# Performance work log

Hardware: AMD Instinct MI355X
Metric: run time of the kernel (lower is better)

Reference implementation:

```python
import jax, jax.numpy as jnp
import numpy as np

NUM_HEADS = 16
ROPE_BASE = 10000.0
QK_GAIN_INIT = 12.0
EPS = 1e-6
# head_config = alternating ['rope','nope',...]; 1.0 -> RoPE applied to this head
ROPE_MASK = jnp.asarray(np.tile([1.0, 0.0], NUM_HEADS // 2), dtype=jnp.float32)


def setup_inputs() -> dict:
    key = jax.random.key(0)
    k0, k1, k2 = jax.random.split(key, 3)
    B, S, Dm = 2, 2048, 2048
    x = jax.random.normal(k0, (B, S, Dm), dtype=jnp.float32)
    # fused QKV projection and output projection (out_proj flagged zero-init in the
    # original; we use small random init so outputs/grads are non-trivial)
    w_qkv = jax.random.normal(k1, (Dm, 3 * Dm), dtype=jnp.float32) * (Dm ** -0.5)
    w_out = jax.random.normal(k2, (Dm, Dm), dtype=jnp.float32) * (Dm ** -0.5)
    q_gain = jnp.full((NUM_HEADS,), QK_GAIN_INIT, dtype=jnp.float32)
    return {"x": x, "w_qkv": w_qkv, "w_out": w_out, "q_gain": q_gain}


def _rope_cos_sin(seqlen, head_dim, dtype):
    half = head_dim // 2
    inv_freq = ROPE_BASE ** (-jnp.arange(0, half, dtype=jnp.float32) / half)
    theta = jnp.arange(seqlen, dtype=jnp.float32)[:, None] * inv_freq[None, :]  # [S, D/2]
    return jnp.cos(theta).astype(dtype), jnp.sin(theta).astype(dtype)


def _apply_rope(t, cos, sin):
    # t: [B, S, H, D]; cos/sin: [S, D/2] -> broadcast [1, S, 1, D/2]
    d2 = t.shape[-1] // 2
    t1, t2 = t[..., :d2], t[..., d2:]
    c = cos[None, :, None, :]
    s = sin[None, :, None, :]
    return jnp.concatenate([t1 * c - t2 * s, t1 * s + t2 * c], axis=-1)


def _unit_norm(t):
    # per-head-dim L2 normalization (qk-norm)
    return t * jax.lax.rsqrt(jnp.sum(t * t, axis=-1, keepdims=True) + EPS)


def reference(x, w_qkv, w_out, q_gain):
    B, S, Dm = x.shape
    H = NUM_HEADS
    D = Dm // H
    qkv = (x @ w_qkv).reshape(B, S, 3, H, D)
    q, k, v = qkv[:, :, 0], qkv[:, :, 1], qkv[:, :, 2]  # [B, S, H, D]
    q = _unit_norm(q)
    k = _unit_norm(k)
    cos, sin = _rope_cos_sin(S, D, x.dtype)
    m = ROPE_MASK[None, None, :, None]  # heterogeneous per-head dispatch
    q = m * _apply_rope(q, cos, sin) + (1.0 - m) * q
    k = m * _apply_rope(k, cos, sin) + (1.0 - m) * k
    # per-head learned qk gain instead of 1/sqrt(d)
    logits = jnp.einsum('bshd,bthd->bhst', q, k) * q_gain[None, :, None, None]
    causal = jnp.tril(jnp.ones((S, S), dtype=bool))
    logits = jnp.where(causal[None, None], logits, jnp.finfo(logits.dtype).min)
    attn = jax.nn.softmax(logits, axis=-1)
    y = jnp.einsum('bhst,bthd->bshd', attn, v).reshape(B, S, Dm)
    return y @ w_out
```

## Files before the change

kernel.cpp:

```cpp
#include <hip/hip_runtime.h>
#include <hip/hip_bf16.h>

typedef unsigned short ushort_t;
typedef __attribute__((ext_vector_type(8))) short short8;
typedef __attribute__((ext_vector_type(4))) float floatx4;

#define B_  2
#define S_  2048
#define DM_ 2048
#define H_  16
#define DH_ 128

#define AS1(p) ((const __attribute__((address_space(1))) void*)(p))
#define AS3(p) ((__attribute__((address_space(3))) void*)(p))

static __device__ __forceinline__ float b2f(ushort_t u) {
  __hip_bfloat16 h = *reinterpret_cast<__hip_bfloat16*>(&u);
  return __bfloat162float(h);
}
static __device__ __forceinline__ ushort_t f2b(float f) {
  __hip_bfloat16 h = __float2bfloat16(f);
  return *reinterpret_cast<ushort_t*>(&h);
}

__global__ __launch_bounds__(256) void convert_f32_bf16(const float* __restrict__ in,
                                                        ushort_t* __restrict__ out) {
  size_t i = ((size_t)blockIdx.x * 256 + threadIdx.x) * 8;
  float4 a = *(const float4*)(in + i);
  float4 b = *(const float4*)(in + i + 4);
  ushort_t tmp[8] = {f2b(a.x), f2b(a.y), f2b(a.z), f2b(a.w),
                     f2b(b.x), f2b(b.y), f2b(b.z), f2b(b.w)};
  *(uint4*)(out + i) = *(const uint4*)tmp;
}

__global__ __launch_bounds__(256) void transpose_f32_to_bf16T(const float* __restrict__ in,
                                                              ushort_t* __restrict__ out,
                                                              int R, int inC, int colOff) {
  __shared__ ushort_t tile[64][72];
  const int tid = threadIdx.x;
  const int r0 = blockIdx.y * 64, c0 = blockIdx.x * 64;
#pragma unroll
  for (int p = 0; p < 2; ++p) {
    int li = tid + p * 256;
    int r = li >> 3, cs = (li & 7) * 8;
    const float* src = in + (size_t)(r0 + r) * inC + colOff + c0 + cs;
    float4 a = *(const float4*)src;
    float4 b = *(const float4*)(src + 4);
    ushort_t tmp[8] = {f2b(a.x), f2b(a.y), f2b(a.z), f2b(a.w),
                       f2b(b.x), f2b(b.y), f2b(b.z), f2b(b.w)};
    *(uint4*)&tile[r][cs] = *(const uint4*)tmp;
  }
  __syncthreads();
#pragma unroll
  for (int p = 0; p < 2; ++p) {
    int li = tid + p * 256;
    int cR = li >> 3, rs = (li & 7) * 8;
    ushort_t tmp[8];
#pragma unroll
    for (int e = 0; e < 8; ++e) tmp[e] = tile[rs + e][cR];
    *(uint4*)(out + (size_t)(c0 + cR) * R + r0 + rs) = *(const uint4*)tmp;
  }
}

template <int MODE>
__global__ __launch_bounds__(256) void gemm_bt_async(const ushort_t* __restrict__ A,
                                                     const ushort_t* __restrict__ Bt,
                                                     void* __restrict__ C0,
                                                     void* __restrict__ C1,
                                                     int M, int N, int K) {
  __shared__ alignas(16) ushort_t As[2][128 * 32];
  __shared__ alignas(16) ushort_t Bs[2][128 * 32];
  const int tid = threadIdx.x;
  const int wave = tid >> 6, lane = tid & 63;
  const int l15 = lane & 15, quad = lane >> 4;
  const int wr = (wave >> 1) * 64, wc = (wave & 1) * 64;
  const int lin = blockIdx.y * gridDim.x + blockIdx.x;
  const int band = lin / (4 * gridDim.x);
  const int rin = lin % (4 * gridDim.x);
  const int by = band * 4 + (rin & 3);
  const int bx = rin >> 2;
  const size_t m0 = (size_t)by * 128, n0 = (size_t)bx * 128;
  const int srow = lane >> 2, scol = (lane & 3) * 8;

  floatx4 zero = {0.f, 0.f, 0.f, 0.f};
  floatx4 acc[4][4];
#pragma unroll
  for (int i = 0; i < 4; ++i)
#pragma unroll
    for (int j = 0; j < 4; ++j) acc[i][j] = zero;

  auto stage = [&](int kt, int bf) {
#pragma unroll
    for (int i = 0; i < 2; ++i) {
      int c = wave * 2 + i;
      int row = c * 16 + srow;
      __builtin_amdgcn_global_load_lds(AS1(A + (m0 + row) * K + kt + scol),
                                       AS3((char*)As[bf] + c * 1024), 16, 0, 0);
      __builtin_amdgcn_global_load_lds(AS1(Bt + (n0 + row) * K + kt + scol),
                                       AS3((char*)Bs[bf] + c * 1024), 16, 0, 0);
    }
  };

  stage(0, 0);
  const int niter = K / 32;
  for (int it = 0; it < niter; ++it) {
    const int cur = it & 1;
    __syncthreads();
    if (it + 1 < niter) stage((it + 1) * 32, cur ^ 1);

    short8 af[4], bfr[4];
#pragma unroll
    for (int i = 0; i < 4; ++i)
      af[i] = *(const short8*)&As[cur][(wr + i * 16 + l15) * 32 + quad * 8];
#pragma unroll
    for (int j = 0; j < 4; ++j)
      bfr[j] = *(const short8*)&Bs[cur][(wc + j * 16 + l15) * 32 + quad * 8];
#pragma unroll
    for (int i = 0; i < 4; ++i)
#pragma unroll
      for (int j = 0; j < 4; ++j)
        acc[i][j] = __builtin_amdgcn_mfma_f32_16x16x32_bf16(af[i], bfr[j], acc[i][j], 0, 0, 0);
  }

#pragma unroll
  for (int i = 0; i < 4; ++i)
#pragma unroll
    for (int j = 0; j < 4; ++j)
#pragma unroll
      for (int r = 0; r < 4; ++r) {
        size_t row = m0 + wr + i * 16 + quad * 4 + r;
        size_t col = n0 + wc + j * 16 + l15;
        if (MODE == 1)
          ((float*)C0)[row * N + col] = acc[i][j][r];
        else
          ((ushort_t*)C0)[row * N + col] = f2b(acc[i][j][r]);
      }
}

#define SBAR() __builtin_amdgcn_sched_barrier(0)
#define BARR() __builtin_amdgcn_s_barrier()

#define LDS_A(qm, bb)                                                          \
  _Pragma("unroll") for (int mi = 0; mi < 4; ++mi) {                           \
    _Pragma("unroll") for (int ks = 0; ks < 2; ++ks) {                         \
      const int r_ = arow + (qm) * 64 + mi * 16;                               \
      const int cb_ = ((ks) * 64 + quad * 16) ^ swz;                           \
      afr[qm][mi][ks] =                                                        \
          *(const short8*)((const char*)As[bb] + r_ * 128 + cb_);              \
    }                                                                          \
  }

#define LDS_B(qn, bb)                                                          \
  _Pragma("unroll") for (int ni = 0; ni < 2; ++ni) {                           \
    _Pragma("unroll") for (int ks = 0; ks < 2; ++ks) {                         \
      const int r_ = brow + (qn) * 32 + ni * 16;                               \
      const int cb_ = ((ks) * 64 + quad * 16) ^ swz;                           \
      bfr[qn][ni][ks] =                                                        \
          *(const short8*)((const char*)Bs[bb] + r_ * 128 + cb_);              \
    }                                                                          \
  }

#define MMA_Q(qm, qn)                                                          \
  _Pragma("unroll") for (int mi = 0; mi < 4; ++mi) {                           \
    _Pragma("unroll") for (int ni = 0; ni < 2; ++ni) {                         \
      floatx4 t_ = acc[(qm) * 4 + mi][(qn) * 2 + ni];                          \
      t_ = __builtin_amdgcn_mfma_f32_16x16x32_bf16(afr[qm][mi][0],             \
                                                   bfr[qn][ni][0], t_, 0, 0, 0); \
      t_ = __builtin_amdgcn_mfma_f32_16x16x32_bf16(afr[qm][mi][1],             \
                                                   bfr[qn][ni][1], t_, 0, 0, 0); \
      acc[(qm) * 4 + mi][(qn) * 2 + ni] = t_;                                  \
    }                                                                          \
  }

template <int MODE>
__global__ __launch_bounds__(512, 2) void gemm_bt_256(const ushort_t* __restrict__ A,
                                                      const ushort_t* __restrict__ Bt,
                                                      void* __restrict__ C0,
                                                      void* __restrict__ C1,
                                                      int M, int N, int K) {
  __shared__ alignas(16) ushort_t As[2][256 * 64];
  __shared__ alignas(16) ushort_t Bs[2][256 * 64];
  const int tid = threadIdx.x;
  const int wave = tid >> 6, lane = tid & 63;
  const int l15 = lane & 15, quad = lane >> 4;
  const int wm = wave >> 2, wn = wave & 3;
  const size_t m0 = (size_t)blockIdx.y * 256, n0 = (size_t)blockIdx.x * 256;
  const int nkt = K >> 6;

  const int srow = lane >> 3;
  const int skk = ((lane & 7) ^ srow) * 8;

  const int arow = wm * 128 + l15;
  const int brow = wn * 64 + l15;
  const int swz = (l15 & 7) << 4;

  floatx4 zero = {0.f, 0.f, 0.f, 0.f};
  floatx4 acc[8][4];
#pragma unroll
  for (int i = 0; i < 8; ++i)
#pragma unroll
    for (int j = 0; j < 4; ++j) acc[i][j] = zero;

  short8 afr[2][4][2];
  short8 bfr[2][2][2];

  auto stage_half = [&](int t, int ht) {
    if (t >= nkt) return;
    const int bb = t & 1;
    const int h = ht & 1;
    const int kt64 = t << 6;
    const ushort_t* G = (ht < 2) ? A : Bt;
    const size_t r0 = (ht < 2) ? m0 : n0;
    char* dst = (char*)((ht < 2) ? As[bb] : Bs[bb]) + h * 16384;
#pragma unroll
    for (int i = 0; i < 2; ++i) {
      const int c = wave * 2 + i;
      const size_t gr = r0 + h * 128 + c * 8 + srow;
      __builtin_amdgcn_global_load_lds(AS1(G + gr * K + kt64 + skk),
                                       AS3(dst + c * 1024), 16, 0, 0);
    }
  };

  stage_half(0, 0); stage_half(0, 1); stage_half(0, 2); stage_half(0, 3);
  stage_half(1, 0); stage_half(1, 1);
  SBAR();
  if (nkt > 1) { asm volatile("s_waitcnt vmcnt(4)" ::: "memory"); }
  else         { asm volatile("s_waitcnt vmcnt(0)" ::: "memory"); }
  SBAR(); BARR(); SBAR();

  for (int kt = 0; kt < nkt; ++kt) {
    const int bb = kt & 1;
    LDS_A(0, bb); LDS_B(0, bb);
    stage_half(kt + 1, 2);
    SBAR(); BARR(); SBAR();
    __builtin_amdgcn_s_setprio(1);
    MMA_Q(0, 0);
    __builtin_amdgcn_s_setprio(0);
    SBAR(); BARR(); SBAR();
    LDS_A(1, bb);
    stage_half(kt + 1, 3);
    SBAR(); BARR(); SBAR();
    __builtin_amdgcn_s_setprio(1);
    MMA_Q(1, 0);
    __builtin_amdgcn_s_setprio(0);
    SBAR(); BARR(); SBAR();
    LDS_B(1, bb);
    stage_half(kt + 2, 0);
    SBAR(); BARR(); SBAR();
    __builtin_amdgcn_s_setprio(1);
    MMA_Q(1, 1);
    __builtin_amdgcn_s_setprio(0);
    SBAR(); BARR(); SBAR();
    stage_half(kt + 2, 1);
    SBAR(); BARR(); SBAR();
    __builtin_amdgcn_s_setprio(1);
    MMA_Q(0, 1);
    __builtin_amdgcn_s_setprio(0);
    SBAR();
    if (kt + 2 < nkt) { asm volatile("s_waitcnt vmcnt(4)" ::: "memory"); }
    else              { asm volatile("s_waitcnt vmcnt(0)" ::: "memory"); }
    SBAR(); BARR(); SBAR();
  }

  if (MODE == 2) {
    ushort_t* Cb = (n0 >= 2048) ? (ushort_t*)C1 : (ushort_t*)C0;
    size_t nc0 = n0 & 2047;
#pragma unroll
    for (int mi8 = 0; mi8 < 8; ++mi8)
#pragma unroll
      for (int nj = 0; nj < 4; ++nj)
#pragma unroll
        for (int r = 0; r < 4; ++r) {
          size_t row = m0 + wm * 128 + (mi8 >> 2) * 64 + (mi8 & 3) * 16 + quad * 4 + r;
          size_t col = nc0 + wn * 64 + (nj >> 1) * 32 + (nj & 1) * 16 + l15;
          Cb[row * 2048 + col] = f2b(acc[mi8][nj][r]);
        }
  } else {
#pragma unroll
    for (int mi8 = 0; mi8 < 8; ++mi8)
#pragma unroll
      for (int nj = 0; nj < 4; ++nj)
#pragma unroll
        for (int r = 0; r < 4; ++r) {
          size_t row = m0 + wm * 128 + (mi8 >> 2) * 64 + (mi8 & 3) * 16 + quad * 4 + r;
          size_t col = n0 + wn * 64 + (nj >> 1) * 32 + (nj & 1) * 16 + l15;
          if (MODE == 1)
            ((float*)C0)[row * N + col] = acc[mi8][nj][r];
          else
            ((ushort_t*)C0)[row * N + col] = f2b(acc[mi8][nj][r]);
        }
  }
}

__global__ __launch_bounds__(256) void norm_rope(ushort_t* __restrict__ Q,
                                                 ushort_t* __restrict__ Kb,
                                                 const float* __restrict__ gain) {
  const int tid = threadIdx.x;
  const int wave = tid >> 6, lane = tid & 63;
  const int idx = blockIdx.x * 4 + wave;
  const int h = idx & 15;
  const int s = (idx >> 4) & (S_ - 1);
  const size_t off = (size_t)(idx >> 4) * DM_ + h * DH_;

  float q1 = b2f(Q[off + lane]),  q2 = b2f(Q[off + 64 + lane]);
  float k1 = b2f(Kb[off + lane]), k2 = b2f(Kb[off + 64 + lane]);

  float sq = q1 * q1 + q2 * q2;
  float sk = k1 * k1 + k2 * k2;
#pragma unroll
  for (int o = 1; o < 64; o <<= 1) {
    sq += __shfl_xor(sq, o, 64);
    sk += __shfl_xor(sk, o, 64);
  }
  float rq = rsqrtf(sq + 1e-6f), rk = rsqrtf(sk + 1e-6f);
  q1 *= rq; q2 *= rq; k1 *= rk; k2 *= rk;

  float qo1 = q1, qo2 = q2, ko1 = k1, ko2 = k2;
  if ((h & 1) == 0) {
    float invf = powf(10000.0f, -(float)lane * (1.0f / 64.0f));
    float th = (float)s * invf;
    float c = cosf(th), sn = sinf(th);
    qo1 = q1 * c - q2 * sn;  qo2 = q1 * sn + q2 * c;
    ko1 = k1 * c - k2 * sn;  ko2 = k1 * sn + k2 * c;
  }
  float g = gain[h];
  qo1 *= g; qo2 *= g;

  Q[off + lane]       = f2b(qo1);
  Q[off + 64 + lane]  = f2b(qo2);
  Kb[off + lane]      = f2b(ko1);
  Kb[off + 64 + lane] = f2b(ko2);
}

__global__ __launch_bounds__(256, 2) void attn(ushort_t* __restrict__ QY,
                                               const ushort_t* __restrict__ Kg,
                                               const ushort_t* __restrict__ Vg) {
  __shared__ alignas(16) ushort_t Ks[2][64 * 128];
  __shared__ alignas(16) ushort_t Vs[2][128 * 64];
  __shared__ alignas(16) ushort_t Ps[2][4][16 * 64];

  const float M0 = 13.0f;
  const int tid = threadIdx.x;
  const int wave = tid >> 6, lane = tid & 63;
  const int l15 = lane & 15, quad = lane >> 4;
  const int bh = blockIdx.y;
  const int b = bh >> 4, h = bh & 15;
  const int p = blockIdx.x;
  const int qt[2] = {p, 31 - p};

  const ushort_t* Kgb = Kg + (size_t)b * S_ * DM_ + h * DH_;
  const ushort_t* Vgb = Vg + (size_t)(h * DH_) * (B_ * S_) + b * S_;

  short8 aq[2][4];
#pragma unroll
  for (int t = 0; t < 2; ++t) {
    const ushort_t* Qg =
        QY + (size_t)(b * S_ + qt[t] * 64 + wave * 16 + l15) * DM_ + h * DH_;
#pragma unroll
    for (int ks = 0; ks < 4; ++ks)
      aq[t][ks] = *(const short8*)(Qg + ks * 32 + quad * 8);
  }

  float lsum[2][4] = {{0.f, 0.f, 0.f, 0.f}, {0.f, 0.f, 0.f, 0.f}};
  floatx4 zero = {0.f, 0.f, 0.f, 0.f};
  floatx4 oacc[2][8];
#pragma unroll
  for (int t = 0; t < 2; ++t)
#pragma unroll
    for (int d = 0; d < 8; ++d) oacc[t][d] = zero;

  const int krow_in = lane >> 4, ksd = lane & 15;
  const int vrow_in = lane >> 3, vsd = lane & 7;

  auto stage = [&](int kt, int bf) {
#pragma unroll
    for (int i = 0; i < 4; ++i) {
      int c = wave * 4 + i;
      {
        int r = c * 4 + krow_in;
        int sg = ksd ^ (r & 7);
        __builtin_amdgcn_global_load_lds(
            AS1(Kgb + (size_t)(kt * 64 + r) * DM_ + sg * 8),
            AS3((char*)Ks[bf] + c * 1024), 16, 0, 0);
      }
      {
        int r = c * 8 + vrow_in;
        int sg = vsd ^ (r & 7);
        __builtin_amdgcn_global_load_lds(
            AS1(Vgb + (size_t)r * (B_ * S_) + kt * 64 + sg * 8),
            AS3((char*)Vs[bf] + c * 1024), 16, 0, 0);
      }
    }
  };

  stage(0, 0);

  for (int kt = 0; kt <= qt[1]; ++kt) {
    const int cur = kt & 1;
    __syncthreads();
    if (kt < qt[1]) stage(kt + 1, cur ^ 1);

#pragma unroll
    for (int t = 0; t < 2; ++t) {
      if (t == 0 && kt > qt[0]) continue;
      floatx4 sacc[4];
#pragma unroll
      for (int j = 0; j < 4; ++j) sacc[j] = zero;
#pragma unroll
      for (int ks = 0; ks < 4; ++ks) {
#pragma unroll
        for (int j = 0; j < 4; ++j) {
          int row = j * 16 + l15;
          int sl = (ks * 4 + quad) ^ (row & 7);
          short8 bk = *(const short8*)&Ks[cur][row * 128 + sl * 8];
          sacc[j] = __builtin_amdgcn_mfma_f32_16x16x32_bf16(aq[t][ks], bk, sacc[j], 0, 0, 0);
        }
      }
      if (kt == qt[t]) {
#pragma unroll
        for (int j = 0; j < 4; ++j)
#pragma unroll
          for (int r = 0; r < 4; ++r) {
            int key = j * 16 + l15;
            int qr = wave * 16 + quad * 4 + r;
            if (key > qr) sacc[j][r] = -1e30f;
          }
      }
#pragma unroll
      for (int j = 0; j < 4; ++j)
#pragma unroll
        for (int r = 0; r < 4; ++r) {
          float pv = __expf(sacc[j][r] - M0);
          sacc[j][r] = pv;
          lsum[t][r] += pv;
        }
#pragma unroll
      for (int j = 0; j < 4; ++j)
#pragma unroll
        for (int r = 0; r < 4; ++r) {
          int row = quad * 4 + r;
          int col = j * 16 + l15;
          int g = col >> 3, w = col & 7;
          Ps[t][wave][row * 64 + ((g ^ (row & 7)) << 3) + w] = f2b(sacc[j][r]);
        }
#pragma unroll
      for (int ks2 = 0; ks2 < 2; ++ks2) {
        short8 ap = *(const short8*)&Ps[t][wave][l15 * 64 +
                                                (((ks2 * 4 + quad) ^ (l15 & 7)) << 3)];
#pragma unroll
        for (int d = 0; d < 8; ++d) {
          int row = d * 16 + l15;
          int sl = (ks2 * 4 + quad) ^ (row & 7);
          short8 bv = *(const short8*)&Vs[cur][row * 64 + sl * 8];
          oacc[t][d] = __builtin_amdgcn_mfma_f32_16x16x32_bf16(ap, bv, oacc[t][d], 0, 0, 0);
        }
      }
    }
  }

#pragma unroll
  for (int t = 0; t < 2; ++t) {
#pragma unroll
    for (int r = 0; r < 4; ++r) {
#pragma unroll
      for (int o = 1; o < 16; o <<= 1) lsum[t][r] += __shfl_xor(lsum[t][r], o, 64);
      float inv = 1.0f / lsum[t][r];
      size_t row = (size_t)(b * S_ + qt[t] * 64 + wave * 16 + quad * 4 + r);
#pragma unroll
      for (int d = 0; d < 8; ++d) {
        size_t col = (size_t)h * DH_ + d * 16 + l15;
        QY[row * DM_ + col] = f2b(oacc[t][d][r] * inv);
      }
    }
  }
}

extern "C" void kernel_launch(void* const* d_in, const int* in_sizes, int n_in,
                              void* d_out, int out_size, void* d_ws, size_t ws_size,
                              hipStream_t stream) {
  const float* x      = (const float*)d_in[0];
  const float* w_qkv  = (const float*)d_in[1];
  const float* w_out  = (const float*)d_in[2];
  const float* q_gain = (const float*)d_in[3];
  float* out = (float*)d_out;

  char* ws = (char*)d_ws;
  const size_t bsd = (size_t)B_ * S_ * DM_;
  ushort_t* Qraw = (ushort_t*)ws;
  ushort_t* Kraw = Qraw + bsd;
  ushort_t* Vt   = Kraw + bsd;
  ushort_t* wvT  = Vt + bsd;
  ushort_t* xbf  = (ushort_t*)d_out;
  ushort_t* wqkT = xbf + bsd;
  ushort_t* woutT = Kraw;

  convert_f32_bf16<<<dim3(bsd / (8 * 256)), 256, 0, stream>>>(x, xbf);
  transpose_f32_to_bf16T<<<dim3(64, 32), 256, 0, stream>>>(w_qkv, wqkT, DM_, 3 * DM_, 0);
  transpose_f32_to_bf16T<<<dim3(32, 32), 256, 0, stream>>>(w_qkv, wvT, DM_, 3 * DM_, 2 * DM_);

  gemm_bt_256<2><<<dim3(16, 16), 512, 0, stream>>>(xbf, wqkT, Qraw, Kraw,
                                                   B_ * S_, 2 * DM_, DM_);
  gemm_bt_async<0><<<dim3(32, 16), 256, 0, stream>>>(wvT, xbf, Vt, nullptr,
                                                     DM_, B_ * S_, DM_);
  norm_rope<<<dim3(B_ * S_ * H_ / 4), 256, 0, stream>>>(Qraw, Kraw, q_gain);
  attn<<<dim3(S_ / 128, B_ * H_), 256, 0, stream>>>(Qraw, Kraw, Vt);
  transpose_f32_to_bf16T<<<dim3(32, 32), 256, 0, stream>>>(w_out, woutT, DM_, DM_, 0);
  gemm_bt_async<1><<<dim3(16, 32), 256, 0, stream>>>(Qraw, woutT, out, nullptr,
                                                     B_ * S_, DM_, DM_);
}
```

Before: 392.4 us.

## Restage GEMM prefetch, vectorize norm_rope, use exp2 softmax, swap attn grid axes

The 256-tile GEMM now issues all four half-tile loads for the next k-step up front, waiting at vmcnt(8), and moves later stages into the third and fourth MMA phases. norm_rope handles four rows per wave with 4-wide vector loads and a 16-lane reduction. The log2(e) factor is folded into the q gain so attention can use a hardware exp2 with a rescaled max constant. The attention grid swaps its x and y axes so that heads sharing a query pair are scheduled next to each other.

```diff
diff --git a/kernel.cpp b/kernel.cpp
--- a/kernel.cpp
+++ b/kernel.cpp
@@ -21,6 +21,17 @@
 static __device__ __forceinline__ ushort_t f2b(float f) {
   __hip_bfloat16 h = __float2bfloat16(f);
   return *reinterpret_cast<ushort_t*>(&h);
+}
+static __device__ __forceinline__ float fast_exp2(float x) {
+#if defined(__has_builtin)
+#if __has_builtin(__builtin_amdgcn_exp2f)
+  return __builtin_amdgcn_exp2f(x);
+#else
+  return exp2f(x);
+#endif
+#else
+  return exp2f(x);
+#endif
 }
 
 __global__ __launch_bounds__(256) void convert_f32_bf16(const float* __restrict__ in,
@@ -222,42 +233,40 @@
   };
 
   stage_half(0, 0); stage_half(0, 1); stage_half(0, 2); stage_half(0, 3);
-  stage_half(1, 0); stage_half(1, 1);
+  stage_half(1, 0); stage_half(1, 1); stage_half(1, 2); stage_half(1, 3);
   SBAR();
-  if (nkt > 1) { asm volatile("s_waitcnt vmcnt(4)" ::: "memory"); }
+  if (nkt > 1) { asm volatile("s_waitcnt vmcnt(8)" ::: "memory"); }
   else         { asm volatile("s_waitcnt vmcnt(0)" ::: "memory"); }
   SBAR(); BARR(); SBAR();
 
   for (int kt = 0; kt < nkt; ++kt) {
     const int bb = kt & 1;
     LDS_A(0, bb); LDS_B(0, bb);
-    stage_half(kt + 1, 2);
     SBAR(); BARR(); SBAR();
     __builtin_amdgcn_s_setprio(1);
     MMA_Q(0, 0);
     __builtin_amdgcn_s_setprio(0);
     SBAR(); BARR(); SBAR();
     LDS_A(1, bb);
-    stage_half(kt + 1, 3);
     SBAR(); BARR(); SBAR();
     __builtin_amdgcn_s_setprio(1);
     MMA_Q(1, 0);
     __builtin_amdgcn_s_setprio(0);
     SBAR(); BARR(); SBAR();
     LDS_B(1, bb);
-    stage_half(kt + 2, 0);
+    stage_half(kt + 2, 0); stage_half(kt + 2, 1);
     SBAR(); BARR(); SBAR();
     __builtin_amdgcn_s_setprio(1);
     MMA_Q(1, 1);
     __builtin_amdgcn_s_setprio(0);
     SBAR(); BARR(); SBAR();
-    stage_half(kt + 2, 1);
+    stage_half(kt + 2, 2); stage_half(kt + 2, 3);
     SBAR(); BARR(); SBAR();
     __builtin_amdgcn_s_setprio(1);
     MMA_Q(0, 1);
     __builtin_amdgcn_s_setprio(0);
     SBAR();
-    if (kt + 2 < nkt) { asm volatile("s_waitcnt vmcnt(4)" ::: "memory"); }
+    if (kt + 2 < nkt) { asm volatile("s_waitcnt vmcnt(8)" ::: "memory"); }
     else              { asm volatile("s_waitcnt vmcnt(0)" ::: "memory"); }
     SBAR(); BARR(); SBAR();
   }
@@ -297,39 +306,55 @@
                                                  const float* __restrict__ gain) {
   const int tid = threadIdx.x;
   const int wave = tid >> 6, lane = tid & 63;
-  const int idx = blockIdx.x * 4 + wave;
+  const int g16 = lane >> 4, sl = lane & 15;
+  const int idx = (blockIdx.x * 4 + wave) * 4 + g16;
   const int h = idx & 15;
   const int s = (idx >> 4) & (S_ - 1);
-  const size_t off = (size_t)(idx >> 4) * DM_ + h * DH_;
-
-  float q1 = b2f(Q[off + lane]),  q2 = b2f(Q[off + 64 + lane]);
-  float k1 = b2f(Kb[off + lane]), k2 = b2f(Kb[off + 64 + lane]);
-
-  float sq = q1 * q1 + q2 * q2;
-  float sk = k1 * k1 + k2 * k2;
-#pragma unroll
-  for (int o = 1; o < 64; o <<= 1) {
+  const size_t off = (size_t)(idx >> 4) * DM_ + h * DH_ + sl * 4;
+
+  ushort_t qv1[4], qv2[4], kv1[4], kv2[4];
+  *(uint2*)qv1 = *(const uint2*)(Q + off);
+  *(uint2*)qv2 = *(const uint2*)(Q + off + 64);
+  *(uint2*)kv1 = *(const uint2*)(Kb + off);
+  *(uint2*)kv2 = *(const uint2*)(Kb + off + 64);
+
+  float q1[4], q2[4], k1[4], k2[4];
+  float sq = 0.f, sk = 0.f;
+#pragma unroll
+  for (int e = 0; e < 4; ++e) {
+    q1[e] = b2f(qv1[e]); q2[e] = b2f(qv2[e]);
+    k1[e] = b2f(kv1[e]); k2[e] = b2f(kv2[e]);
+    sq += q1[e] * q1[e] + q2[e] * q2[e];
+    sk += k1[e] * k1[e] + k2[e] * k2[e];
+  }
+#pragma unroll
+  for (int o = 1; o < 16; o <<= 1) {
     sq += __shfl_xor(sq, o, 64);
     sk += __shfl_xor(sk, o, 64);
   }
   float rq = rsqrtf(sq + 1e-6f), rk = rsqrtf(sk + 1e-6f);
-  q1 *= rq; q2 *= rq; k1 *= rk; k2 *= rk;
-
-  float qo1 = q1, qo2 = q2, ko1 = k1, ko2 = k2;
-  if ((h & 1) == 0) {
-    float invf = powf(10000.0f, -(float)lane * (1.0f / 64.0f));
-    float th = (float)s * invf;
-    float c = cosf(th), sn = sinf(th);
-    qo1 = q1 * c - q2 * sn;  qo2 = q1 * sn + q2 * c;
-    ko1 = k1 * c - k2 * sn;  ko2 = k1 * sn + k2 * c;
-  }
-  float g = gain[h];
-  qo1 *= g; qo2 *= g;
-
-  Q[off + lane]       = f2b(qo1);
-  Q[off + 64 + lane]  = f2b(qo2);
-  Kb[off + lane]      = f2b(ko1);
-  Kb[off + 64 + lane] = f2b(ko2);
+  const float g = gain[h] * 1.44269504f;
+  const bool roped = (h & 1) == 0;
+#pragma unroll
+  for (int e = 0; e < 4; ++e) {
+    float a = q1[e] * rq, bq = q2[e] * rq;
+    float c_ = k1[e] * rk, dk = k2[e] * rk;
+    if (roped) {
+      int j = sl * 4 + e;
+      float invf = exp2f((float)j * -0.20762050593f);
+      float th = (float)s * invf;
+      float cc = cosf(th), sn = sinf(th);
+      float na = a * cc - bq * sn, nb = a * sn + bq * cc;
+      float nc = c_ * cc - dk * sn, nd = c_ * sn + dk * cc;
+      a = na; bq = nb; c_ = nc; dk = nd;
+    }
+    qv1[e] = f2b(a * g); qv2[e] = f2b(bq * g);
+    kv1[e] = f2b(c_);    kv2[e] = f2b(dk);
+  }
+  *(uint2*)(Q + off)       = *(const uint2*)qv1;
+  *(uint2*)(Q + off + 64)  = *(const uint2*)qv2;
+  *(uint2*)(Kb + off)      = *(const uint2*)kv1;
+  *(uint2*)(Kb + off + 64) = *(const uint2*)kv2;
 }
 
 __global__ __launch_bounds__(256, 2) void attn(ushort_t* __restrict__ QY,
@@ -339,13 +364,13 @@
   __shared__ alignas(16) ushort_t Vs[2][128 * 64];
   __shared__ alignas(16) ushort_t Ps[2][4][16 * 64];
 
-  const float M0 = 13.0f;
+  const float M0 = 18.755035531f;
   const int tid = threadIdx.x;
   const int wave = tid >> 6, lane = tid & 63;
   const int l15 = lane & 15, quad = lane >> 4;
-  const int bh = blockIdx.y;
+  const int bh = blockIdx.x;
   const int b = bh >> 4, h = bh & 15;
-  const int p = blockIdx.x;
+  const int p = blockIdx.y;
   const int qt[2] = {p, 31 - p};
 
   const ushort_t* Kgb = Kg + (size_t)b * S_ * DM_ + h * DH_;
@@ -430,7 +455,7 @@
       for (int j = 0; j < 4; ++j)
 #pragma unroll
         for (int r = 0; r < 4; ++r) {
-          float pv = __expf(sacc[j][r] - M0);
+          float pv = fast_exp2(sacc[j][r] - M0);
           sacc[j][r] = pv;
           lsum[t][r] += pv;
         }
@@ -502,8 +527,8 @@
                                                    B_ * S_, 2 * DM_, DM_);
   gemm_bt_async<0><<<dim3(32, 16), 256, 0, stream>>>(wvT, xbf, Vt, nullptr,
                                                      DM_, B_ * S_, DM_);
-  norm_rope<<<dim3(B_ * S_ * H_ / 4), 256, 0, stream>>>(Qraw, Kraw, q_gain);
-  attn<<<dim3(S_ / 128, B_ * H_), 256, 0, stream>>>(Qraw, Kraw, Vt);
+  norm_rope<<<dim3(B_ * S_ * H_ / 16), 256, 0, stream>>>(Qraw, Kraw, q_gain);
+  attn<<<dim3(B_ * H_, S_ / 128), 256, 0, stream>>>(Qraw, Kraw, Vt);
   transpose_f32_to_bf16T<<<dim3(32, 32), 256, 0, stream>>>(w_out, woutT, DM_, DM_, 0);
   gemm_bt_async<1><<<dim3(16, 32), 256, 0, stream>>>(Qraw, woutT, out, nullptr,
                                                      B_ * S_, DM_, DM_);
```

After: 372.7 us. -5.0%, faster.
